# Kernel optimization log

Hardware: AMD Instinct MI355X
Metric: run time of the kernel (lower is better)

## Reference

```python
import jax, jax.numpy as jnp
import numpy as np

B, S, DM = 8, 1024, 512   # batch, seq_len, model dim
H, D = 8, 64              # n_heads, per-head dim


def setup_inputs() -> dict:
    key = jax.random.key(0)
    k1, k2, k3, k4, k5 = jax.random.split(key, 5)
    sc = 1.0 / np.sqrt(DM)
    return {
        "x": jax.random.normal(k1, (B, S, DM), dtype=jnp.float32),
        "Wq": jax.random.normal(k2, (H, DM, D), dtype=jnp.float32) * sc,
        "Wk": jax.random.normal(k3, (H, DM, D), dtype=jnp.float32) * sc,
        "Wv": jax.random.normal(k4, (H, DM, D), dtype=jnp.float32) * sc,
        "Wo": jax.random.normal(k5, (H * D, DM), dtype=jnp.float32) * (1.0 / np.sqrt(H * D)),
    }


def reference(x, Wq, Wk, Wv, Wo):
    # Batched multi-head attention equivalent to the per-head Python loop.
    q = jnp.einsum("bsm,hmd->bhsd", x, Wq)
    k = jnp.einsum("bsm,hmd->bhsd", x, Wk)
    v = jnp.einsum("bsm,hmd->bhsd", x, Wv)
    scores = jnp.einsum("bhsd,bhtd->bhst", q, k) / jnp.sqrt(jnp.float32(D))
    attn = jax.nn.softmax(scores, axis=-1)          # [B,H,S,S]
    heads = jnp.einsum("bhst,bhtd->bhsd", attn, v)  # [B,H,S,D]
    # concat heads along feature dim (head order matches loop order)
    concat = heads.transpose(0, 2, 1, 3).reshape(B, S, H * D)
    z = jnp.einsum("bsf,fm->bsm", concat, Wo)       # output projection
    return z, attn
```

## Files before the change

kernel.cpp:

```cpp
#include <hip/hip_runtime.h>

#define B 8
#define S 1024
#define DM 512
#define H 8
#define D 64

typedef __attribute__((ext_vector_type(8))) short bf16x8;
typedef __attribute__((ext_vector_type(4))) float f32x4;

__device__ inline f32x4 mfma16(bf16x8 a, bf16x8 b, f32x4 c) {
  return __builtin_amdgcn_mfma_f32_16x16x32_bf16(a, b, c, 0, 0, 0);
}

__device__ inline ushort f2bf(float f) {
  uint u = __float_as_uint(f);
  u += 0x7fff + ((u >> 16) & 1);
  return (ushort)(u >> 16);
}

__device__ inline float bf2f(ushort u) {
  return __uint_as_float(((uint)u) << 16);
}

__global__ __launch_bounds__(256) void cast_x_kernel(const float* __restrict__ x,
                                                     ushort* __restrict__ xbf) {
  int idx = blockIdx.x * 256 + threadIdx.x;
  float4 v = *(const float4*)(x + (size_t)idx * 4);
  ushort4 o;
  o.x = f2bf(v.x); o.y = f2bf(v.y); o.z = f2bf(v.z); o.w = f2bf(v.w);
  *(ushort4*)(xbf + (size_t)idx * 4) = o;
}

__global__ __launch_bounds__(256) void prep_w_kernel(
    const float* __restrict__ Wq, const float* __restrict__ Wk,
    const float* __restrict__ Wv, const float* __restrict__ Wo,
    ushort* __restrict__ WT, ushort* __restrict__ WoT) {
  int idx = blockIdx.x * 256 + threadIdx.x;
  if (idx < 1536 * 512) {
    int f = idx >> 9, m = idx & 511;
    int g = f >> 9, fl = f & 511, h = fl >> 6, d = fl & 63;
    const float* W = (g == 0) ? Wq : (g == 1) ? Wk : Wv;
    WT[idx] = f2bf(W[((size_t)h * DM + m) * D + d]);
  } else {
    int i2 = idx - 1536 * 512;
    int m = i2 >> 9, f = i2 & 511;
    WoT[(size_t)m * 512 + f] = f2bf(Wo[(size_t)f * DM + m]);
  }
}

__global__ __launch_bounds__(256) void qkv_gemm_kernel(
    const ushort* __restrict__ A, const ushort* __restrict__ Bm,
    ushort* __restrict__ qb, ushort* __restrict__ kb, ushort* __restrict__ vt) {
  __shared__ ushort As[64][72], Bs[64][72];
  const int tid = threadIdx.x;
  const int m0 = blockIdx.x * 64, n0 = blockIdx.y * 64;
  const int w = tid >> 6, l = tid & 63;
  const int r = l & 15, q = l >> 4;
  const int mh = (w >> 1) * 32, nh = (w & 1) * 32;

  f32x4 acc[2][2] = {};
  const int srow = tid >> 2, sco = (tid & 3) * 16;

  for (int k0 = 0; k0 < 512; k0 += 64) {
    const ushort* ap = A + (size_t)(m0 + srow) * 512 + k0 + sco;
    const ushort* bp = Bm + (size_t)(n0 + srow) * 512 + k0 + sco;
    uint4 a0 = *(const uint4*)ap;
    uint4 a1 = *(const uint4*)(ap + 8);
    uint4 b0 = *(const uint4*)bp;
    uint4 b1 = *(const uint4*)(bp + 8);
    __syncthreads();
    *(uint4*)&As[srow][sco] = a0;
    *(uint4*)&As[srow][sco + 8] = a1;
    *(uint4*)&Bs[srow][sco] = b0;
    *(uint4*)&Bs[srow][sco + 8] = b1;
    __syncthreads();
    #pragma unroll
    for (int kk = 0; kk < 64; kk += 32) {
      bf16x8 fa0 = *(const bf16x8*)&As[mh + r][kk + q * 8];
      bf16x8 fa1 = *(const bf16x8*)&As[mh + 16 + r][kk + q * 8];
      bf16x8 fb0 = *(const bf16x8*)&Bs[nh + r][kk + q * 8];
      bf16x8 fb1 = *(const bf16x8*)&Bs[nh + 16 + r][kk + q * 8];
      acc[0][0] = mfma16(fa0, fb0, acc[0][0]);
      acc[0][1] = mfma16(fa0, fb1, acc[0][1]);
      acc[1][0] = mfma16(fa1, fb0, acc[1][0]);
      acc[1][1] = mfma16(fa1, fb1, acc[1][1]);
    }
  }

  const int g = n0 >> 9;
  #pragma unroll
  for (int mi = 0; mi < 2; ++mi)
    #pragma unroll
    for (int nj = 0; nj < 2; ++nj)
      #pragma unroll
      for (int i = 0; i < 4; ++i) {
        int row = m0 + mh + mi * 16 + q * 4 + i;
        int col = n0 + nh + nj * 16 + r;
        int bb = row >> 10, s = row & 1023;
        int fl = col & 511, h = fl >> 6, d = fl & 63;
        ushort val = f2bf(acc[mi][nj][i]);
        if (g == 0)
          qb[(((size_t)bb * H + h) * S + s) * D + d] = val;
        else if (g == 1)
          kb[(((size_t)bb * H + h) * S + s) * D + d] = val;
        else
          vt[(((size_t)bb * H + h) * D + d) * S + s] = val;
      }
}

__global__ __launch_bounds__(256, 4) void attn_kernel(
    const ushort* __restrict__ qb, const ushort* __restrict__ kb,
    const ushort* __restrict__ vt, float* __restrict__ attn,
    ushort* __restrict__ concat) {
  __shared__ ushort Pl[16 * 1024];
  __shared__ float redm[4][16], redsum[4][16];
  __shared__ float rinvL[16];
  const int tid = threadIdx.x;
  const int w = tid >> 6, l = tid & 63;
  const int r = l & 15, q = l >> 4;

  const int n = blockIdx.x;
  const int rank = n >> 3;
  const int bh = (n & 7) * 8 + (rank >> 6);
  const int s0 = (rank & 63) * 16;

  const ushort* qp = qb + ((size_t)bh * S + s0) * D;
  bf16x8 qa0 = *(const bf16x8*)(qp + r * 64 + q * 8);
  bf16x8 qa1 = *(const bf16x8*)(qp + r * 64 + 32 + q * 8);

  const ushort* kp = kb + (size_t)bh * S * D;
  f32x4 sc[16];
  #pragma unroll
  for (int kt = 0; kt < 16; ++kt) {
    const ushort* kr = kp + (size_t)(w * 256 + kt * 16 + r) * 64 + q * 8;
    bf16x8 kf0 = *(const bf16x8*)kr;
    bf16x8 kf1 = *(const bf16x8*)(kr + 32);
    f32x4 a = {};
    a = mfma16(qa0, kf0, a);
    a = mfma16(qa1, kf1, a);
    sc[kt] = a * 0.125f;
  }

  float mx[4];
  #pragma unroll
  for (int i = 0; i < 4; ++i) {
    float m = sc[0][i];
    #pragma unroll
    for (int kt = 1; kt < 16; ++kt) m = fmaxf(m, sc[kt][i]);
    #pragma unroll
    for (int msk = 1; msk < 16; msk <<= 1) m = fmaxf(m, __shfl_xor(m, msk));
    mx[i] = m;
  }
  if (r == 0) {
    #pragma unroll
    for (int i = 0; i < 4; ++i) redm[w][q * 4 + i] = mx[i];
  }
  __syncthreads();
  #pragma unroll
  for (int i = 0; i < 4; ++i)
    mx[i] = fmaxf(fmaxf(redm[0][q * 4 + i], redm[1][q * 4 + i]),
                  fmaxf(redm[2][q * 4 + i], redm[3][q * 4 + i]));

  float sm[4] = {0.f, 0.f, 0.f, 0.f};
  #pragma unroll
  for (int kt = 0; kt < 16; ++kt)
    #pragma unroll
    for (int i = 0; i < 4; ++i) {
      float e = __expf(sc[kt][i] - mx[i]);
      sc[kt][i] = e;
      sm[i] += e;
    }
  #pragma unroll
  for (int i = 0; i < 4; ++i) {
    float s = sm[i];
    #pragma unroll
    for (int msk = 1; msk < 16; msk <<= 1) s += __shfl_xor(s, msk);
    sm[i] = s;
  }
  if (r == 0) {
    #pragma unroll
    for (int i = 0; i < 4; ++i) redsum[w][q * 4 + i] = sm[i];
  }
  __syncthreads();
  float rinv[4];
  #pragma unroll
  for (int i = 0; i < 4; ++i)
    rinv[i] = 1.0f / (redsum[0][q * 4 + i] + redsum[1][q * 4 + i] +
                      redsum[2][q * 4 + i] + redsum[3][q * 4 + i]);
  if (w == 0 && r == 0) {
    #pragma unroll
    for (int i = 0; i < 4; ++i) rinvL[q * 4 + i] = rinv[i];
  }

  #pragma unroll
  for (int kt = 0; kt < 16; ++kt) {
    int col = w * 256 + kt * 16 + r;
    #pragma unroll
    for (int i = 0; i < 4; ++i) {
      int row = q * 4 + i;
      Pl[row * 1024 + (col ^ ((row & 7) << 3))] = f2bf(sc[kt][i]);
    }
  }
  __syncthreads();

  {
    const int d0 = w * 16;
    const ushort* vp = vt + ((size_t)bh * D + d0 + r) * S;
    f32x4 acc[4] = {};
    #pragma unroll
    for (int stp = 0; stp < 32; ++stp) {
      int t0 = stp * 32 + q * 8;
      bf16x8 pa = *(const bf16x8*)&Pl[r * 1024 + (t0 ^ ((r & 7) << 3))];
      bf16x8 vb = *(const bf16x8*)(vp + t0);
      acc[stp & 3] = mfma16(pa, vb, acc[stp & 3]);
    }
    f32x4 tot = acc[0] + acc[1] + acc[2] + acc[3];
    const int b = bh >> 3, h = bh & 7;
    #pragma unroll
    for (int i = 0; i < 4; ++i)
      concat[((size_t)b * S + s0 + q * 4 + i) * DM + h * D + d0 + r] =
          f2bf(tot[i] * rinv[i]);
  }

  {
    float* ap = attn + ((size_t)bh * S + s0) * S;
    #pragma unroll
    for (int uu = 0; uu < 16; ++uu) {
      const int row = w * 4 + (uu >> 2);
      const int chunk = uu & 3;
      const int c = chunk * 256 + l * 4;
      const int swz = (row & 7) << 3;
      ushort4 p4 = *(const ushort4*)&Pl[row * 1024 + (c ^ swz)];
      const float rv = rinvL[row];
      f32x4 o;
      o.x = bf2f(p4.x) * rv;
      o.y = bf2f(p4.y) * rv;
      o.z = bf2f(p4.z) * rv;
      o.w = bf2f(p4.w) * rv;
      __builtin_nontemporal_store(
          o, (f32x4*)(ap + (size_t)row * S + c));
    }
  }
}

__global__ __launch_bounds__(256) void outproj_gemm_kernel(
    const ushort* __restrict__ A, const ushort* __restrict__ Bm,
    float* __restrict__ z) {
  __shared__ ushort As[64][72], Bs[64][72];
  const int tid = threadIdx.x;
  const int m0 = blockIdx.x * 64, n0 = blockIdx.y * 64;
  const int w = tid >> 6, l = tid & 63;
  const int r = l & 15, q = l >> 4;
  const int mh = (w >> 1) * 32, nh = (w & 1) * 32;

  f32x4 acc[2][2] = {};
  const int srow = tid >> 2, sco = (tid & 3) * 16;

  for (int k0 = 0; k0 < 512; k0 += 64) {
    const ushort* ap = A + (size_t)(m0 + srow) * 512 + k0 + sco;
    const ushort* bp = Bm + (size_t)(n0 + srow) * 512 + k0 + sco;
    uint4 a0 = *(const uint4*)ap;
    uint4 a1 = *(const uint4*)(ap + 8);
    uint4 b0 = *(const uint4*)bp;
    uint4 b1 = *(const uint4*)(bp + 8);
    __syncthreads();
    *(uint4*)&As[srow][sco] = a0;
    *(uint4*)&As[srow][sco + 8] = a1;
    *(uint4*)&Bs[srow][sco] = b0;
    *(uint4*)&Bs[srow][sco + 8] = b1;
    __syncthreads();
    #pragma unroll
    for (int kk = 0; kk < 64; kk += 32) {
      bf16x8 fa0 = *(const bf16x8*)&As[mh + r][kk + q * 8];
      bf16x8 fa1 = *(const bf16x8*)&As[mh + 16 + r][kk + q * 8];
      bf16x8 fb0 = *(const bf16x8*)&Bs[nh + r][kk + q * 8];
      bf16x8 fb1 = *(const bf16x8*)&Bs[nh + 16 + r][kk + q * 8];
      acc[0][0] = mfma16(fa0, fb0, acc[0][0]);
      acc[0][1] = mfma16(fa0, fb1, acc[0][1]);
      acc[1][0] = mfma16(fa1, fb0, acc[1][0]);
      acc[1][1] = mfma16(fa1, fb1, acc[1][1]);
    }
  }

  #pragma unroll
  for (int mi = 0; mi < 2; ++mi)
    #pragma unroll
    for (int nj = 0; nj < 2; ++nj)
      #pragma unroll
      for (int i = 0; i < 4; ++i) {
        int row = m0 + mh + mi * 16 + q * 4 + i;
        int col = n0 + nh + nj * 16 + r;
        z[(size_t)row * DM + col] = acc[mi][nj][i];
      }
}

extern "C" void kernel_launch(void* const* d_in, const int* in_sizes, int n_in,
                              void* d_out, int out_size, void* d_ws, size_t ws_size,
                              hipStream_t stream) {
  const float* x  = (const float*)d_in[0];
  const float* Wq = (const float*)d_in[1];
  const float* Wk = (const float*)d_in[2];
  const float* Wv = (const float*)d_in[3];
  const float* Wo = (const float*)d_in[4];

  float* z    = (float*)d_out;
  float* attn = z + (size_t)B * S * DM;

  ushort* xbf    = (ushort*)d_ws;
  ushort* WT     = xbf + (size_t)8192 * 512;
  ushort* WoT    = WT + (size_t)1536 * 512;
  ushort* qb     = WoT + (size_t)512 * 512;
  ushort* kb     = qb + (size_t)B * H * S * D;
  ushort* vt     = kb + (size_t)B * H * S * D;
  ushort* concat = vt + (size_t)B * H * S * D;

  cast_x_kernel<<<(B * S * DM / 4 + 255) / 256, 256, 0, stream>>>(x, xbf);
  prep_w_kernel<<<(1536 * 512 + 512 * 512) / 256, 256, 0, stream>>>(
      Wq, Wk, Wv, Wo, WT, WoT);
  qkv_gemm_kernel<<<dim3(8192 / 64, 1536 / 64), 256, 0, stream>>>(
      xbf, WT, qb, kb, vt);
  attn_kernel<<<4096, 256, 0, stream>>>(
      qb, kb, vt, attn, concat);
  outproj_gemm_kernel<<<dim3(8192 / 64, 512 / 64), 256, 0, stream>>>(
      concat, WoT, z);
}
```

Before: 186.6 us.

## Use 8 waves per attention block with single-sync online softmax merge

Doubles the attention block to 512 threads so each wave computes scores for 128 keys instead of 256. The softmax now computes each wave's local max and sum and merges them with exponential correction, which removes one barrier. After the shared-memory barrier, waves 0-3 do the P·V MFMA while waves 4-7 write the fp32 attention matrix, so the two run concurrently. V fragments are prefetched before the barrier. The cost is a higher thread count per block and more shared reduction arrays, which may change occupancy.

```diff
diff --git a/kernel.cpp b/kernel.cpp
--- a/kernel.cpp
+++ b/kernel.cpp
@@ -109,12 +109,12 @@
       }
 }
 
-__global__ __launch_bounds__(256, 4) void attn_kernel(
+__global__ __launch_bounds__(512, 6) void attn_v3(
     const ushort* __restrict__ qb, const ushort* __restrict__ kb,
     const ushort* __restrict__ vt, float* __restrict__ attn,
     ushort* __restrict__ concat) {
   __shared__ ushort Pl[16 * 1024];
-  __shared__ float redm[4][16], redsum[4][16];
+  __shared__ float redm[8][16], redsum[8][16];
   __shared__ float rinvL[16];
   const int tid = threadIdx.x;
   const int w = tid >> 6, l = tid & 63;
@@ -130,10 +130,10 @@
   bf16x8 qa1 = *(const bf16x8*)(qp + r * 64 + 32 + q * 8);
 
   const ushort* kp = kb + (size_t)bh * S * D;
-  f32x4 sc[16];
-  #pragma unroll
-  for (int kt = 0; kt < 16; ++kt) {
-    const ushort* kr = kp + (size_t)(w * 256 + kt * 16 + r) * 64 + q * 8;
+  f32x4 sc[8];
+  #pragma unroll
+  for (int kt = 0; kt < 8; ++kt) {
+    const ushort* kr = kp + (size_t)(w * 128 + kt * 16 + r) * 64 + q * 8;
     bf16x8 kf0 = *(const bf16x8*)kr;
     bf16x8 kf1 = *(const bf16x8*)(kr + 32);
     f32x4 a = {};
@@ -142,92 +142,102 @@
     sc[kt] = a * 0.125f;
   }
 
-  float mx[4];
+  float mxl[4];
   #pragma unroll
   for (int i = 0; i < 4; ++i) {
     float m = sc[0][i];
     #pragma unroll
-    for (int kt = 1; kt < 16; ++kt) m = fmaxf(m, sc[kt][i]);
+    for (int kt = 1; kt < 8; ++kt) m = fmaxf(m, sc[kt][i]);
     #pragma unroll
     for (int msk = 1; msk < 16; msk <<= 1) m = fmaxf(m, __shfl_xor(m, msk));
-    mx[i] = m;
+    mxl[i] = m;
+  }
+
+  float sml[4] = {0.f, 0.f, 0.f, 0.f};
+  #pragma unroll
+  for (int kt = 0; kt < 8; ++kt)
+    #pragma unroll
+    for (int i = 0; i < 4; ++i) {
+      float e = __expf(sc[kt][i] - mxl[i]);
+      sc[kt][i] = e;
+      sml[i] += e;
+    }
+  #pragma unroll
+  for (int i = 0; i < 4; ++i) {
+    float s = sml[i];
+    #pragma unroll
+    for (int msk = 1; msk < 16; msk <<= 1) s += __shfl_xor(s, msk);
+    sml[i] = s;
   }
   if (r == 0) {
     #pragma unroll
-    for (int i = 0; i < 4; ++i) redm[w][q * 4 + i] = mx[i];
+    for (int i = 0; i < 4; ++i) {
+      redm[w][q * 4 + i] = mxl[i];
+      redsum[w][q * 4 + i] = sml[i];
+    }
   }
   __syncthreads();
-  #pragma unroll
-  for (int i = 0; i < 4; ++i)
-    mx[i] = fmaxf(fmaxf(redm[0][q * 4 + i], redm[1][q * 4 + i]),
-                  fmaxf(redm[2][q * 4 + i], redm[3][q * 4 + i]));
-
-  float sm[4] = {0.f, 0.f, 0.f, 0.f};
-  #pragma unroll
-  for (int kt = 0; kt < 16; ++kt)
-    #pragma unroll
-    for (int i = 0; i < 4; ++i) {
-      float e = __expf(sc[kt][i] - mx[i]);
-      sc[kt][i] = e;
-      sm[i] += e;
-    }
+
+  float rinv[4], corr[4];
   #pragma unroll
   for (int i = 0; i < 4; ++i) {
-    float s = sm[i];
-    #pragma unroll
-    for (int msk = 1; msk < 16; msk <<= 1) s += __shfl_xor(s, msk);
-    sm[i] = s;
-  }
-  if (r == 0) {
-    #pragma unroll
-    for (int i = 0; i < 4; ++i) redsum[w][q * 4 + i] = sm[i];
-  }
-  __syncthreads();
-  float rinv[4];
-  #pragma unroll
-  for (int i = 0; i < 4; ++i)
-    rinv[i] = 1.0f / (redsum[0][q * 4 + i] + redsum[1][q * 4 + i] +
-                      redsum[2][q * 4 + i] + redsum[3][q * 4 + i]);
+    const int rr = q * 4 + i;
+    float m = redm[0][rr];
+    #pragma unroll
+    for (int ww = 1; ww < 8; ++ww) m = fmaxf(m, redm[ww][rr]);
+    float tot = 0.f;
+    #pragma unroll
+    for (int ww = 0; ww < 8; ++ww)
+      tot += redsum[ww][rr] * __expf(redm[ww][rr] - m);
+    rinv[i] = 1.0f / tot;
+    corr[i] = __expf(mxl[i] - m);
+  }
   if (w == 0 && r == 0) {
     #pragma unroll
     for (int i = 0; i < 4; ++i) rinvL[q * 4 + i] = rinv[i];
   }
 
-  #pragma unroll
-  for (int kt = 0; kt < 16; ++kt) {
-    int col = w * 256 + kt * 16 + r;
+  const ushort* vp = vt + ((size_t)bh * D + (w & 3) * 16 + r) * S;
+  bf16x8 vpre[4];
+  if (w < 4) {
+    #pragma unroll
+    for (int pp = 0; pp < 4; ++pp)
+      vpre[pp] = *(const bf16x8*)(vp + pp * 32 + q * 8);
+  }
+
+  #pragma unroll
+  for (int kt = 0; kt < 8; ++kt) {
+    int col = w * 128 + kt * 16 + r;
     #pragma unroll
     for (int i = 0; i < 4; ++i) {
       int row = q * 4 + i;
-      Pl[row * 1024 + (col ^ ((row & 7) << 3))] = f2bf(sc[kt][i]);
+      Pl[row * 1024 + (col ^ ((row & 7) << 3))] = f2bf(sc[kt][i] * corr[i]);
     }
   }
   __syncthreads();
 
-  {
-    const int d0 = w * 16;
-    const ushort* vp = vt + ((size_t)bh * D + d0 + r) * S;
+  if (w < 4) {
     f32x4 acc[4] = {};
     #pragma unroll
     for (int stp = 0; stp < 32; ++stp) {
       int t0 = stp * 32 + q * 8;
       bf16x8 pa = *(const bf16x8*)&Pl[r * 1024 + (t0 ^ ((r & 7) << 3))];
-      bf16x8 vb = *(const bf16x8*)(vp + t0);
+      bf16x8 vb = (stp < 4) ? vpre[stp] : *(const bf16x8*)(vp + t0);
       acc[stp & 3] = mfma16(pa, vb, acc[stp & 3]);
     }
     f32x4 tot = acc[0] + acc[1] + acc[2] + acc[3];
     const int b = bh >> 3, h = bh & 7;
+    const int d0 = w * 16;
     #pragma unroll
     for (int i = 0; i < 4; ++i)
       concat[((size_t)b * S + s0 + q * 4 + i) * DM + h * D + d0 + r] =
           f2bf(tot[i] * rinv[i]);
-  }
-
-  {
+  } else {
+    const int ws = w - 4;
     float* ap = attn + ((size_t)bh * S + s0) * S;
     #pragma unroll
     for (int uu = 0; uu < 16; ++uu) {
-      const int row = w * 4 + (uu >> 2);
+      const int row = ws * 4 + (uu >> 2);
       const int chunk = uu & 3;
       const int c = chunk * 256 + l * 4;
       const int swz = (row & 7) << 3;
@@ -238,8 +248,7 @@
       o.y = bf2f(p4.y) * rv;
       o.z = bf2f(p4.z) * rv;
       o.w = bf2f(p4.w) * rv;
-      __builtin_nontemporal_store(
-          o, (f32x4*)(ap + (size_t)row * S + c));
+      __builtin_nontemporal_store(o, (f32x4*)(ap + (size_t)row * S + c));
     }
   }
 }
@@ -320,8 +329,7 @@
       Wq, Wk, Wv, Wo, WT, WoT);
   qkv_gemm_kernel<<<dim3(8192 / 64, 1536 / 64), 256, 0, stream>>>(
       xbf, WT, qb, kb, vt);
-  attn_kernel<<<4096, 256, 0, stream>>>(
-      qb, kb, vt, attn, concat);
+  attn_v3<<<4096, 512, 0, stream>>>(qb, kb, vt, attn, concat);
   outproj_gemm_kernel<<<dim3(8192 / 64, 512 / 64), 256, 0, stream>>>(
       concat, WoT, z);
 }
```

New measurement: 195.0 us. 4.5% more time.

## Use 8 waves per attention block and split PV and attn-store across waves

Applied to the files above, without the earlier changes.

Doubles the attention block to 512 threads so each wave computes scores for 128 keys instead of 256, which halves the per-thread score registers. After softmax, waves 0-3 do the P·V product and write concat while waves 4-7 stream the normalized attention matrix to global memory at the same time. The intent is higher occupancy and overlap of the large attn write with the PV MFMA work. The cost is larger cross-wave reductions through shared memory and a launch bound that may constrain register allocation.

```diff
diff --git a/kernel.cpp b/kernel.cpp
--- a/kernel.cpp
+++ b/kernel.cpp
@@ -109,12 +109,12 @@
       }
 }
 
-__global__ __launch_bounds__(256, 4) void attn_kernel(
+__global__ __launch_bounds__(512, 6) void attn_kernel(
     const ushort* __restrict__ qb, const ushort* __restrict__ kb,
     const ushort* __restrict__ vt, float* __restrict__ attn,
     ushort* __restrict__ concat) {
   __shared__ ushort Pl[16 * 1024];
-  __shared__ float redm[4][16], redsum[4][16];
+  __shared__ float redm[8][16], redsum[8][16];
   __shared__ float rinvL[16];
   const int tid = threadIdx.x;
   const int w = tid >> 6, l = tid & 63;
@@ -130,10 +130,10 @@
   bf16x8 qa1 = *(const bf16x8*)(qp + r * 64 + 32 + q * 8);
 
   const ushort* kp = kb + (size_t)bh * S * D;
-  f32x4 sc[16];
-  #pragma unroll
-  for (int kt = 0; kt < 16; ++kt) {
-    const ushort* kr = kp + (size_t)(w * 256 + kt * 16 + r) * 64 + q * 8;
+  f32x4 sc[8];
+  #pragma unroll
+  for (int kt = 0; kt < 8; ++kt) {
+    const ushort* kr = kp + (size_t)(w * 128 + kt * 16 + r) * 64 + q * 8;
     bf16x8 kf0 = *(const bf16x8*)kr;
     bf16x8 kf1 = *(const bf16x8*)(kr + 32);
     f32x4 a = {};
@@ -147,7 +147,7 @@
   for (int i = 0; i < 4; ++i) {
     float m = sc[0][i];
     #pragma unroll
-    for (int kt = 1; kt < 16; ++kt) m = fmaxf(m, sc[kt][i]);
+    for (int kt = 1; kt < 8; ++kt) m = fmaxf(m, sc[kt][i]);
     #pragma unroll
     for (int msk = 1; msk < 16; msk <<= 1) m = fmaxf(m, __shfl_xor(m, msk));
     mx[i] = m;
@@ -158,13 +158,18 @@
   }
   __syncthreads();
   #pragma unroll
-  for (int i = 0; i < 4; ++i)
-    mx[i] = fmaxf(fmaxf(redm[0][q * 4 + i], redm[1][q * 4 + i]),
-                  fmaxf(redm[2][q * 4 + i], redm[3][q * 4 + i]));
+  for (int i = 0; i < 4; ++i) {
+    int rr = q * 4 + i;
+    float m = fmaxf(fmaxf(redm[0][rr], redm[1][rr]),
+                    fmaxf(redm[2][rr], redm[3][rr]));
+    m = fmaxf(m, fmaxf(fmaxf(redm[4][rr], redm[5][rr]),
+                       fmaxf(redm[6][rr], redm[7][rr])));
+    mx[i] = m;
+  }
 
   float sm[4] = {0.f, 0.f, 0.f, 0.f};
   #pragma unroll
-  for (int kt = 0; kt < 16; ++kt)
+  for (int kt = 0; kt < 8; ++kt)
     #pragma unroll
     for (int i = 0; i < 4; ++i) {
       float e = __expf(sc[kt][i] - mx[i]);
@@ -185,17 +190,20 @@
   __syncthreads();
   float rinv[4];
   #pragma unroll
-  for (int i = 0; i < 4; ++i)
-    rinv[i] = 1.0f / (redsum[0][q * 4 + i] + redsum[1][q * 4 + i] +
-                      redsum[2][q * 4 + i] + redsum[3][q * 4 + i]);
+  for (int i = 0; i < 4; ++i) {
+    int rr = q * 4 + i;
+    float s = (redsum[0][rr] + redsum[1][rr]) + (redsum[2][rr] + redsum[3][rr]) +
+              (redsum[4][rr] + redsum[5][rr]) + (redsum[6][rr] + redsum[7][rr]);
+    rinv[i] = 1.0f / s;
+  }
   if (w == 0 && r == 0) {
     #pragma unroll
     for (int i = 0; i < 4; ++i) rinvL[q * 4 + i] = rinv[i];
   }
 
   #pragma unroll
-  for (int kt = 0; kt < 16; ++kt) {
-    int col = w * 256 + kt * 16 + r;
+  for (int kt = 0; kt < 8; ++kt) {
+    int col = w * 128 + kt * 16 + r;
     #pragma unroll
     for (int i = 0; i < 4; ++i) {
       int row = q * 4 + i;
@@ -204,7 +212,7 @@
   }
   __syncthreads();
 
-  {
+  if (w < 4) {
     const int d0 = w * 16;
     const ushort* vp = vt + ((size_t)bh * D + d0 + r) * S;
     f32x4 acc[4] = {};
@@ -221,13 +229,12 @@
     for (int i = 0; i < 4; ++i)
       concat[((size_t)b * S + s0 + q * 4 + i) * DM + h * D + d0 + r] =
           f2bf(tot[i] * rinv[i]);
-  }
-
-  {
+  } else {
+    const int ws = w - 4;
     float* ap = attn + ((size_t)bh * S + s0) * S;
     #pragma unroll
     for (int uu = 0; uu < 16; ++uu) {
-      const int row = w * 4 + (uu >> 2);
+      const int row = ws * 4 + (uu >> 2);
       const int chunk = uu & 3;
       const int c = chunk * 256 + l * 4;
       const int swz = (row & 7) << 3;
@@ -238,8 +245,7 @@
       o.y = bf2f(p4.y) * rv;
       o.z = bf2f(p4.z) * rv;
       o.w = bf2f(p4.w) * rv;
-      __builtin_nontemporal_store(
-          o, (f32x4*)(ap + (size_t)row * S + c));
+      __builtin_nontemporal_store(o, (f32x4*)(ap + (size_t)row * S + c));
     }
   }
 }
@@ -320,8 +326,7 @@
       Wq, Wk, Wv, Wo, WT, WoT);
   qkv_gemm_kernel<<<dim3(8192 / 64, 1536 / 64), 256, 0, stream>>>(
       xbf, WT, qb, kb, vt);
-  attn_kernel<<<4096, 256, 0, stream>>>(
-      qb, kb, vt, attn, concat);
+  attn_kernel<<<4096, 512, 0, stream>>>(qb, kb, vt, attn, concat);
   outproj_gemm_kernel<<<dim3(8192 / 64, 512 / 64), 256, 0, stream>>>(
       concat, WoT, z);
 }
```

Result: slower. 194.4 us (+4.2%).
